# Kernel optimization log

Hardware: AMD Instinct MI355X
Metric: run time of the kernel (lower is better)

## Reference

```python
import jax, jax.numpy as jnp
import numpy as np

# Normalizer hyperparameters (from init_kwargs)
THETA = 0.3     # final temperature theta
THETA0 = 4.0    # initial annealing temperature
T = 20          # number of annealing iterations
BETA = 0.7      # temperature decay
P = 0.1         # fraction -> k = p * (# finite entries per row)
TEMPERATURE = 1.0

BSZ, SEQ = 4096, 8192


def setup_inputs() -> dict:
    key = jax.random.key(0)
    k1, k2 = jax.random.split(key)
    score = jax.random.normal(k1, (BSZ, SEQ), dtype=jnp.float32)
    mask = jax.random.randint(k2, (BSZ, SEQ), 0, 2, dtype=jnp.int32)
    return {"score": score, "mask": mask}


def reference(score, mask):
    # score: [bsz, seq], mask: [bsz, seq] (0 = masked out)
    score = score * TEMPERATURE
    score = jnp.where(mask == 0, -jnp.inf, score)

    # k = p * number of finite (unmasked) entries per row
    k = jnp.sum(jnp.isfinite(score), axis=-1, keepdims=True).astype(score.dtype) * P

    # annealed temperature schedule: theta_t = max(beta^t * theta0, theta)
    thetas = [max(BETA ** t * THETA0, THETA) for t in range(T)]

    a = jnp.zeros((score.shape[0], 1), dtype=score.dtype)
    b = jnp.zeros_like(score)
    for th in thetas:
        # masked entries: exp(-inf)=0, relu(-inf)=0 -> they contribute nothing
        s = jnp.sum(jnp.exp((score + b) / th), axis=-1, keepdims=True)  # [bsz,1]
        a = th * jnp.log(k / (s + 1e-20))                               # [bsz,1]
        b = -jax.nn.relu(score + a)                                     # [bsz,seq]

    gamma = jnp.exp((score + a + b) / THETA)  # [bsz, seq]
    return gamma
```

## Files before the change

kernel.cpp:

```cpp
#include <hip/hip_runtime.h>
#include <math.h>

#define SEQ      8192
#define NTHREADS 256
#define VPT      32
#define F4PT     8
#define RPB      2

__device__ __forceinline__ float wave_sum(float x) {
    #pragma unroll
    for (int off = 32; off > 0; off >>= 1)
        x += __shfl_xor(x, off, 64);
    return x;
}

__global__ __launch_bounds__(NTHREADS) void normalizer_kernel(
        const float* __restrict__ score,
        const int*   __restrict__ mask,
        float*       __restrict__ out)
{
    const int row0 = blockIdx.x * RPB;
    const int tid  = threadIdx.x;
    const int wid  = tid >> 6;
    const int lane = tid & 63;

    constexpr double L2E = 1.4426950408889634;
    const float cf = (float)(L2E / 0.3);

    const float4* __restrict__ sA = (const float4*)(score + (size_t)row0 * SEQ);
    const int4*   __restrict__ mA = (const int4*)(mask  + (size_t)row0 * SEQ);
    const float4* __restrict__ sB = (const float4*)(score + (size_t)(row0 + 1) * SEQ);
    const int4*   __restrict__ mB = (const int4*)(mask  + (size_t)(row0 + 1) * SEQ);

    float wA[VPT], wB[VPT];
    int cntA = 0, cntB = 0;
    #pragma unroll
    for (int j = 0; j < F4PT; ++j) {
        float4 s = sA[j * NTHREADS + tid];
        int4   m = mA[j * NTHREADS + tid];
        wA[4*j+0] = m.x ? s.x * cf : -INFINITY;
        wA[4*j+1] = m.y ? s.y * cf : -INFINITY;
        wA[4*j+2] = m.z ? s.z * cf : -INFINITY;
        wA[4*j+3] = m.w ? s.w * cf : -INFINITY;
        cntA += (m.x != 0) + (m.y != 0) + (m.z != 0) + (m.w != 0);
    }
    #pragma unroll
    for (int j = 0; j < F4PT; ++j) {
        float4 s = sB[j * NTHREADS + tid];
        int4   m = mB[j * NTHREADS + tid];
        wB[4*j+0] = m.x ? s.x * cf : -INFINITY;
        wB[4*j+1] = m.y ? s.y * cf : -INFINITY;
        wB[4*j+2] = m.z ? s.z * cf : -INFINITY;
        wB[4*j+3] = m.w ? s.w * cf : -INFINITY;
        cntB += (m.x != 0) + (m.y != 0) + (m.z != 0) + (m.w != 0);
    }

    __shared__ float red[21][RPB][4];

    float pA = wave_sum((float)cntA);
    float pB = wave_sum((float)cntB);
    if (lane == 0) { red[0][0][wid] = pA; red[0][1][wid] = pB; }
    __syncthreads();
    const float kA = 0.1f * (red[0][0][0] + red[0][0][1] + red[0][0][2] + red[0][0][3]);
    const float kB = 0.1f * (red[0][1][0] + red[0][1][1] + red[0][1][2] + red[0][1][3]);
    const float l2kA = __builtin_amdgcn_logf(kA);
    const float l2kB = __builtin_amdgcn_logf(kB);
    const float rkA  = 1.0f / kA;
    const float rkB  = 1.0f / kB;

    float NAa = INFINITY, NAb = INFINITY;

    double thd = 4.0;
    #pragma unroll
    for (int t = 0; t < 8; ++t) {
        const float cp  = (float)(0.3 / thd);
        const float inv = (float)(thd / 0.3);
        float a0 = 0.f, a1 = 0.f, b0 = 0.f, b1 = 0.f;
        #pragma unroll
        for (int j = 0; j < VPT; j += 2) {
            a0 += __builtin_amdgcn_exp2f(fminf(wA[j],   NAa) * cp);
            a1 += __builtin_amdgcn_exp2f(fminf(wA[j+1], NAa) * cp);
            b0 += __builtin_amdgcn_exp2f(fminf(wB[j],   NAb) * cp);
            b1 += __builtin_amdgcn_exp2f(fminf(wB[j+1], NAb) * cp);
        }
        float pa = wave_sum(a0 + a1);
        float pb = wave_sum(b0 + b1);
        if (lane == 0) { red[1+t][0][wid] = pa; red[1+t][1][wid] = pb; }
        __syncthreads();
        const float sA_ = red[1+t][0][0] + red[1+t][0][1] + red[1+t][0][2] + red[1+t][0][3];
        const float sB_ = red[1+t][1][0] + red[1+t][1][1] + red[1+t][1][2] + red[1+t][1][3];
        NAa = inv * (__builtin_amdgcn_logf(sA_ + 1e-20f) - l2kA);
        NAb = inv * (__builtin_amdgcn_logf(sB_ + 1e-20f) - l2kB);
        thd *= 0.7;
    }

    #pragma unroll
    for (int j = 0; j < VPT; ++j) {
        wA[j] = __builtin_amdgcn_exp2f(wA[j]);
        wB[j] = __builtin_amdgcn_exp2f(wB[j]);
    }
    float eNAa = __builtin_amdgcn_exp2f(NAa);
    float eNAb = __builtin_amdgcn_exp2f(NAb);

    #pragma unroll
    for (int t = 8; t < 20; ++t) {
        float a0 = 0.f, a1 = 0.f, b0 = 0.f, b1 = 0.f;
        #pragma unroll
        for (int j = 0; j < VPT; j += 2) {
            a0 += fminf(wA[j],   eNAa);
            a1 += fminf(wA[j+1], eNAa);
            b0 += fminf(wB[j],   eNAb);
            b1 += fminf(wB[j+1], eNAb);
        }
        float pa = wave_sum(a0 + a1);
        float pb = wave_sum(b0 + b1);
        if (lane == 0) { red[1+t][0][wid] = pa; red[1+t][1][wid] = pb; }
        __syncthreads();
        const float sA_ = red[1+t][0][0] + red[1+t][0][1] + red[1+t][0][2] + red[1+t][0][3];
        const float sB_ = red[1+t][1][0] + red[1+t][1][1] + red[1+t][1][2] + red[1+t][1][3];
        eNAa = (sA_ + 1e-20f) * rkA;
        eNAb = (sB_ + 1e-20f) * rkB;
    }

    const float ra = 1.0f / eNAa;
    const float rb = 1.0f / eNAb;
    float4* __restrict__ oA = (float4*)(out + (size_t)row0 * SEQ);
    float4* __restrict__ oB = (float4*)(out + (size_t)(row0 + 1) * SEQ);
    #pragma unroll
    for (int j = 0; j < F4PT; ++j) {
        float4 g;
        g.x = fminf(wA[4*j+0], eNAa) * ra;
        g.y = fminf(wA[4*j+1], eNAa) * ra;
        g.z = fminf(wA[4*j+2], eNAa) * ra;
        g.w = fminf(wA[4*j+3], eNAa) * ra;
        oA[j * NTHREADS + tid] = g;
        float4 h;
        h.x = fminf(wB[4*j+0], eNAb) * rb;
        h.y = fminf(wB[4*j+1], eNAb) * rb;
        h.z = fminf(wB[4*j+2], eNAb) * rb;
        h.w = fminf(wB[4*j+3], eNAb) * rb;
        oB[j * NTHREADS + tid] = h;
    }
}

extern "C" void kernel_launch(void* const* d_in, const int* in_sizes, int n_in,
                              void* d_out, int out_size, void* d_ws, size_t ws_size,
                              hipStream_t stream) {
    const float* score = (const float*)d_in[0];
    const int*   mask  = (const int*)d_in[1];
    float*       out   = (float*)d_out;
    const int rows = in_sizes[0] / SEQ;
    normalizer_kernel<<<rows / RPB, NTHREADS, 0, stream>>>(score, mask, out);
}
```

Measured before the change: 340.8 us.

## Process one row per block with incrementally rescaled scores and occupancy hint

Switches from two rows per block to one row per block, which halves the register array per thread, and adds a launch_bounds hint for 8 blocks per CU to raise occupancy. The per-iteration multiply by the temperature ratio is replaced by rescaling the stored scores by 1/0.7 in place. The first iteration is specialized because b=0 there. The shared reduction buffer becomes double-buffered with parity indexing, and the annealing loops are no longer fully unrolled. The risk is losing the ILP from interleaving two rows, plus a small extra multiply pass over the scores in each early iteration.

```diff
diff --git a/kernel.cpp b/kernel.cpp
--- a/kernel.cpp
+++ b/kernel.cpp
@@ -5,7 +5,6 @@
 #define NTHREADS 256
 #define VPT      32
 #define F4PT     8
-#define RPB      2
 
 __device__ __forceinline__ float wave_sum(float x) {
     #pragma unroll
@@ -14,132 +13,116 @@
     return x;
 }
 
-__global__ __launch_bounds__(NTHREADS) void normalizer_kernel(
+__global__ __launch_bounds__(NTHREADS, 8) void normalizer_kernel(
         const float* __restrict__ score,
         const int*   __restrict__ mask,
         float*       __restrict__ out)
 {
-    const int row0 = blockIdx.x * RPB;
+    const int row  = blockIdx.x;
     const int tid  = threadIdx.x;
     const int wid  = tid >> 6;
     const int lane = tid & 63;
 
     constexpr double L2E = 1.4426950408889634;
-    const float cf = (float)(L2E / 0.3);
+    constexpr double TH7 = 4.0*0.7*0.7*0.7*0.7*0.7*0.7*0.7;
+    const float cu0 = (float)(L2E / 4.0);
+    const float r07 = (float)(1.0 / 0.7);
+    const float ce  = (float)(TH7 / 0.3);
 
-    const float4* __restrict__ sA = (const float4*)(score + (size_t)row0 * SEQ);
-    const int4*   __restrict__ mA = (const int4*)(mask  + (size_t)row0 * SEQ);
-    const float4* __restrict__ sB = (const float4*)(score + (size_t)(row0 + 1) * SEQ);
-    const int4*   __restrict__ mB = (const int4*)(mask  + (size_t)(row0 + 1) * SEQ);
+    const float4* __restrict__ s4 = (const float4*)(score + (size_t)row * SEQ);
+    const int4*   __restrict__ m4 = (const int4*)(mask  + (size_t)row * SEQ);
 
-    float wA[VPT], wB[VPT];
-    int cntA = 0, cntB = 0;
+    float u[VPT];
+    int cnt = 0;
     #pragma unroll
     for (int j = 0; j < F4PT; ++j) {
-        float4 s = sA[j * NTHREADS + tid];
-        int4   m = mA[j * NTHREADS + tid];
-        wA[4*j+0] = m.x ? s.x * cf : -INFINITY;
-        wA[4*j+1] = m.y ? s.y * cf : -INFINITY;
-        wA[4*j+2] = m.z ? s.z * cf : -INFINITY;
-        wA[4*j+3] = m.w ? s.w * cf : -INFINITY;
-        cntA += (m.x != 0) + (m.y != 0) + (m.z != 0) + (m.w != 0);
-    }
-    #pragma unroll
-    for (int j = 0; j < F4PT; ++j) {
-        float4 s = sB[j * NTHREADS + tid];
-        int4   m = mB[j * NTHREADS + tid];
-        wB[4*j+0] = m.x ? s.x * cf : -INFINITY;
-        wB[4*j+1] = m.y ? s.y * cf : -INFINITY;
-        wB[4*j+2] = m.z ? s.z * cf : -INFINITY;
-        wB[4*j+3] = m.w ? s.w * cf : -INFINITY;
-        cntB += (m.x != 0) + (m.y != 0) + (m.z != 0) + (m.w != 0);
+        float4 s = s4[j * NTHREADS + tid];
+        int4   m = m4[j * NTHREADS + tid];
+        u[4*j+0] = m.x ? s.x * cu0 : -INFINITY;
+        u[4*j+1] = m.y ? s.y * cu0 : -INFINITY;
+        u[4*j+2] = m.z ? s.z * cu0 : -INFINITY;
+        u[4*j+3] = m.w ? s.w * cu0 : -INFINITY;
+        cnt += (m.x != 0) + (m.y != 0) + (m.z != 0) + (m.w != 0);
     }
 
-    __shared__ float red[21][RPB][4];
+    __shared__ float redc[4];
+    __shared__ float red[2][4];
 
-    float pA = wave_sum((float)cntA);
-    float pB = wave_sum((float)cntB);
-    if (lane == 0) { red[0][0][wid] = pA; red[0][1][wid] = pB; }
+    float a0 = 0.f, a1 = 0.f;
+    #pragma unroll
+    for (int j = 0; j < VPT; j += 2) {
+        a0 += __builtin_amdgcn_exp2f(u[j]);
+        a1 += __builtin_amdgcn_exp2f(u[j+1]);
+    }
+    float pc = wave_sum((float)cnt);
+    float ps = wave_sum(a0 + a1);
+    if (lane == 0) { redc[wid] = pc; red[0][wid] = ps; }
+    #pragma unroll
+    for (int j = 0; j < VPT; ++j) u[j] *= r07;
     __syncthreads();
-    const float kA = 0.1f * (red[0][0][0] + red[0][0][1] + red[0][0][2] + red[0][0][3]);
-    const float kB = 0.1f * (red[0][1][0] + red[0][1][1] + red[0][1][2] + red[0][1][3]);
-    const float l2kA = __builtin_amdgcn_logf(kA);
-    const float l2kB = __builtin_amdgcn_logf(kB);
-    const float rkA  = 1.0f / kA;
-    const float rkB  = 1.0f / kB;
+    const float k   = 0.1f * (redc[0] + redc[1] + redc[2] + redc[3]);
+    const float l2k = __builtin_amdgcn_logf(k);
+    const float rk  = 1.0f / k;
+    float s_ = red[0][0] + red[0][1] + red[0][2] + red[0][3];
+    float NAcp = (__builtin_amdgcn_logf(s_ + 1e-20f) - l2k) * r07;
 
-    float NAa = INFINITY, NAb = INFINITY;
-
-    double thd = 4.0;
-    #pragma unroll
-    for (int t = 0; t < 8; ++t) {
-        const float cp  = (float)(0.3 / thd);
-        const float inv = (float)(thd / 0.3);
-        float a0 = 0.f, a1 = 0.f, b0 = 0.f, b1 = 0.f;
+    for (int t = 1; t < 7; ++t) {
+        a0 = 0.f; a1 = 0.f;
         #pragma unroll
         for (int j = 0; j < VPT; j += 2) {
-            a0 += __builtin_amdgcn_exp2f(fminf(wA[j],   NAa) * cp);
-            a1 += __builtin_amdgcn_exp2f(fminf(wA[j+1], NAa) * cp);
-            b0 += __builtin_amdgcn_exp2f(fminf(wB[j],   NAb) * cp);
-            b1 += __builtin_amdgcn_exp2f(fminf(wB[j+1], NAb) * cp);
+            a0 += __builtin_amdgcn_exp2f(fminf(u[j],   NAcp));
+            a1 += __builtin_amdgcn_exp2f(fminf(u[j+1], NAcp));
         }
         float pa = wave_sum(a0 + a1);
-        float pb = wave_sum(b0 + b1);
-        if (lane == 0) { red[1+t][0][wid] = pa; red[1+t][1][wid] = pb; }
+        if (lane == 0) red[t & 1][wid] = pa;
+        #pragma unroll
+        for (int j = 0; j < VPT; ++j) u[j] *= r07;
         __syncthreads();
-        const float sA_ = red[1+t][0][0] + red[1+t][0][1] + red[1+t][0][2] + red[1+t][0][3];
-        const float sB_ = red[1+t][1][0] + red[1+t][1][1] + red[1+t][1][2] + red[1+t][1][3];
-        NAa = inv * (__builtin_amdgcn_logf(sA_ + 1e-20f) - l2kA);
-        NAb = inv * (__builtin_amdgcn_logf(sB_ + 1e-20f) - l2kB);
-        thd *= 0.7;
+        s_ = red[t & 1][0] + red[t & 1][1] + red[t & 1][2] + red[t & 1][3];
+        NAcp = (__builtin_amdgcn_logf(s_ + 1e-20f) - l2k) * r07;
     }
 
-    #pragma unroll
-    for (int j = 0; j < VPT; ++j) {
-        wA[j] = __builtin_amdgcn_exp2f(wA[j]);
-        wB[j] = __builtin_amdgcn_exp2f(wB[j]);
-    }
-    float eNAa = __builtin_amdgcn_exp2f(NAa);
-    float eNAb = __builtin_amdgcn_exp2f(NAb);
-
-    #pragma unroll
-    for (int t = 8; t < 20; ++t) {
-        float a0 = 0.f, a1 = 0.f, b0 = 0.f, b1 = 0.f;
+    {
+        a0 = 0.f; a1 = 0.f;
         #pragma unroll
         for (int j = 0; j < VPT; j += 2) {
-            a0 += fminf(wA[j],   eNAa);
-            a1 += fminf(wA[j+1], eNAa);
-            b0 += fminf(wB[j],   eNAb);
-            b1 += fminf(wB[j+1], eNAb);
+            a0 += __builtin_amdgcn_exp2f(fminf(u[j],   NAcp));
+            a1 += __builtin_amdgcn_exp2f(fminf(u[j+1], NAcp));
         }
         float pa = wave_sum(a0 + a1);
-        float pb = wave_sum(b0 + b1);
-        if (lane == 0) { red[1+t][0][wid] = pa; red[1+t][1][wid] = pb; }
+        if (lane == 0) red[1][wid] = pa;
+        #pragma unroll
+        for (int j = 0; j < VPT; ++j)
+            u[j] = __builtin_amdgcn_exp2f(u[j] * ce);
         __syncthreads();
-        const float sA_ = red[1+t][0][0] + red[1+t][0][1] + red[1+t][0][2] + red[1+t][0][3];
-        const float sB_ = red[1+t][1][0] + red[1+t][1][1] + red[1+t][1][2] + red[1+t][1][3];
-        eNAa = (sA_ + 1e-20f) * rkA;
-        eNAb = (sB_ + 1e-20f) * rkB;
+        s_ = red[1][0] + red[1][1] + red[1][2] + red[1][3];
+    }
+    float eNA = __builtin_amdgcn_exp2f((__builtin_amdgcn_logf(s_ + 1e-20f) - l2k) * ce);
+
+    for (int t = 8; t < 20; ++t) {
+        a0 = 0.f; a1 = 0.f;
+        #pragma unroll
+        for (int j = 0; j < VPT; j += 2) {
+            a0 += fminf(u[j],   eNA);
+            a1 += fminf(u[j+1], eNA);
+        }
+        float pa = wave_sum(a0 + a1);
+        if (lane == 0) red[t & 1][wid] = pa;
+        __syncthreads();
+        s_ = red[t & 1][0] + red[t & 1][1] + red[t & 1][2] + red[t & 1][3];
+        eNA = (s_ + 1e-20f) * rk;
     }
 
-    const float ra = 1.0f / eNAa;
-    const float rb = 1.0f / eNAb;
-    float4* __restrict__ oA = (float4*)(out + (size_t)row0 * SEQ);
-    float4* __restrict__ oB = (float4*)(out + (size_t)(row0 + 1) * SEQ);
+    const float ra = 1.0f / eNA;
+    float4* __restrict__ o4 = (float4*)(out + (size_t)row * SEQ);
     #pragma unroll
     for (int j = 0; j < F4PT; ++j) {
         float4 g;
-        g.x = fminf(wA[4*j+0], eNAa) * ra;
-        g.y = fminf(wA[4*j+1], eNAa) * ra;
-        g.z = fminf(wA[4*j+2], eNAa) * ra;
-        g.w = fminf(wA[4*j+3], eNAa) * ra;
-        oA[j * NTHREADS + tid] = g;
-        float4 h;
-        h.x = fminf(wB[4*j+0], eNAb) * rb;
-        h.y = fminf(wB[4*j+1], eNAb) * rb;
-        h.z = fminf(wB[4*j+2], eNAb) * rb;
-        h.w = fminf(wB[4*j+3], eNAb) * rb;
-        oB[j * NTHREADS + tid] = h;
+        g.x = fminf(u[4*j+0], eNA) * ra;
+        g.y = fminf(u[4*j+1], eNA) * ra;
+        g.z = fminf(u[4*j+2], eNA) * ra;
+        g.w = fminf(u[4*j+3], eNA) * ra;
+        o4[j * NTHREADS + tid] = g;
     }
 }
 
@@ -150,5 +133,5 @@
     const int*   mask  = (const int*)d_in[1];
     float*       out   = (float*)d_out;
     const int rows = in_sizes[0] / SEQ;
-    normalizer_kernel<<<rows / RPB, NTHREADS, 0, stream>>>(score, mask, out);
+    normalizer_kernel<<<rows, NTHREADS, 0, stream>>>(score, mask, out);
 }
```

Result: faster. 329.6 us (-3.3%).
